# Optimization experiments

Hardware: AMD Instinct MI355X
Metric: run time of the kernel (lower is better)

Reference implementation:

```python
import jax, jax.numpy as jnp
import numpy as np
from jax import lax

B, L, ENC_IN, MARK = 8, 512, 7, 4
D_MODEL, EXPAND, D_STATE, D_CONV = 512, 2, 16, 4
D_INNER = D_MODEL * EXPAND
DT_RANK = int(np.ceil(D_MODEL / 16))  # 32
PRED_LEN, C_OUT = 96, 7


def _positional_embedding(seq_len, d_model):
    pos = jnp.arange(seq_len, dtype=jnp.float32)[:, None]
    div = jnp.exp(jnp.arange(0, d_model, 2, dtype=jnp.float32) * (-np.log(10000.0) / d_model))
    pe = jnp.zeros((seq_len, d_model), dtype=jnp.float32)
    pe = pe.at[:, 0::2].set(jnp.sin(pos * div))
    pe = pe.at[:, 1::2].set(jnp.cos(pos * div))
    return pe  # [L, d_model]


def setup_inputs() -> dict:
    key = jax.random.key(0)
    ks = jax.random.split(key, 20)
    s = 0.02
    inp = {
        "x_enc": jax.random.normal(ks[0], (B, L, ENC_IN), jnp.float32),
        "x_mark_enc": jax.random.normal(ks[1], (B, L, MARK), jnp.float32),
        "x_dec": jax.random.normal(ks[2], (B, 144, ENC_IN), jnp.float32),
        "x_mark_dec": jax.random.normal(ks[3], (B, 144, MARK), jnp.float32),
        # DataEmbedding params
        "token_conv_w": jax.random.normal(ks[4], (D_MODEL, ENC_IN, 3), jnp.float32) * s,
        "temporal_w": jax.random.normal(ks[5], (D_MODEL, MARK), jnp.float32) * s,
        # Mamba params
        "in_proj_w": jax.random.normal(ks[6], (2 * D_INNER, D_MODEL), jnp.float32) * s,
        "conv1d_w": jax.random.normal(ks[7], (D_INNER, 1, D_CONV), jnp.float32) * s,
        "conv1d_b": jnp.zeros((D_INNER,), jnp.float32),
        "x_proj_w": jax.random.normal(ks[8], (DT_RANK + 2 * D_STATE, D_INNER), jnp.float32) * s,
        "dt_proj_w": jax.random.normal(ks[9], (D_INNER, DT_RANK), jnp.float32) * s,
        "dt_proj_b": jax.random.normal(ks[10], (D_INNER,), jnp.float32) * s,
        "A_log": jnp.log(jnp.broadcast_to(jnp.arange(1, D_STATE + 1, dtype=jnp.float32), (D_INNER, D_STATE))),
        "D_param": jnp.ones((D_INNER,), jnp.float32),
        "out_proj_w": jax.random.normal(ks[11], (D_MODEL, D_INNER), jnp.float32) * s,
        # prediction head
        "head_w": jax.random.normal(ks[12], (PRED_LEN * C_OUT, D_MODEL), jnp.float32) * s,
        "head_b": jnp.zeros((PRED_LEN * C_OUT,), jnp.float32),
    }
    return inp


def reference(x_enc, x_mark_enc, x_dec, x_mark_dec, token_conv_w, temporal_w,
              in_proj_w, conv1d_w, conv1d_b, x_proj_w, dt_proj_w, dt_proj_b,
              A_log, D_param, out_proj_w, head_w, head_b):
    # --- instance normalization (mean/std detached as in torch) ---
    mean_enc = lax.stop_gradient(jnp.mean(x_enc, axis=1, keepdims=True))       # [B,1,C]
    xc = x_enc - mean_enc
    std_enc = lax.stop_gradient(jnp.sqrt(jnp.var(xc, axis=1, keepdims=True) + 1e-5))
    xn = xc / std_enc                                                          # [B,L,C]

    # --- DataEmbedding: circular conv token emb + timeF linear + sinusoidal PE ---
    xp = jnp.pad(xn, ((0, 0), (1, 1), (0, 0)), mode="wrap")                    # circular pad on L
    val = lax.conv_general_dilated(xp.transpose(0, 2, 1), token_conv_w, (1,), "VALID")  # [B,D,L]
    val = val.transpose(0, 2, 1)                                               # [B,L,D]
    temp = x_mark_enc @ temporal_w.T                                           # [B,L,D]
    x = val + temp + _positional_embedding(L, D_MODEL)[None]                   # [B,L,D]

    # --- Mamba block ---
    xz = x @ in_proj_w.T                                                       # [B,L,2*Di]
    x_part, z = jnp.split(xz, 2, axis=-1)
    # causal depthwise conv over time
    xt = jnp.pad(x_part.transpose(0, 2, 1), ((0, 0), (0, 0), (D_CONV - 1, 0)))
    xconv = lax.conv_general_dilated(xt, conv1d_w, (1,), "VALID",
                                     feature_group_count=D_INNER) + conv1d_b[None, :, None]
    u = jax.nn.silu(xconv.transpose(0, 2, 1))                                  # [B,L,Di]

    dbl = u @ x_proj_w.T                                                       # [B,L,dt_rank+2n]
    dt_low = dbl[..., :DT_RANK]
    Bm = dbl[..., DT_RANK:DT_RANK + D_STATE]                                   # [B,L,n]
    Cm = dbl[..., DT_RANK + D_STATE:]                                          # [B,L,n]
    dt = jax.nn.softplus(dt_low @ dt_proj_w.T + dt_proj_b)                     # [B,L,Di]

    A = -jnp.exp(A_log)                                                        # [Di,n]
    deltaA = jnp.exp(dt[..., None] * A)                                        # [B,L,Di,n]
    deltaBu = dt[..., None] * Bm[:, :, None, :] * u[..., None]                 # [B,L,Di,n]

    def step(h, inputs):
        dA_t, dBu_t, c_t = inputs                                              # [B,Di,n],[B,Di,n],[B,n]
        h = dA_t * h + dBu_t
        y_t = jnp.einsum("bdn,bn->bd", h, c_t)
        return h, y_t

    h0 = jnp.zeros((B, D_INNER, D_STATE), dtype=x.dtype)
    _, ys = lax.scan(step, h0, (deltaA.transpose(1, 0, 2, 3),
                                deltaBu.transpose(1, 0, 2, 3),
                                Cm.transpose(1, 0, 2)))
    y = ys.transpose(1, 0, 2) + u * D_param                                    # [B,L,Di]
    y = y * jax.nn.silu(z)
    x_out = y @ out_proj_w.T                                                   # [B,L,D]

    # --- prediction head on last hidden state ---
    last = x_out[:, -1, :]                                                     # [B,D]
    pred = (last @ head_w.T + head_b).reshape(-1, PRED_LEN, C_OUT)
    return pred * std_enc + mean_enc
```

## Files before the change

### kernel.cpp

```cpp
#include <hip/hip_runtime.h>
#include <hip/hip_bf16.h>
#include <math.h>

#define BB 8
#define LL 512
#define CIN 7
#define MARKN 4
#define DM 512
#define DI 1024
#define DSN 16
#define NOUTC 672
#define NTC 8

typedef unsigned short ushortT;
typedef __attribute__((ext_vector_type(8))) short short8v;
typedef __attribute__((ext_vector_type(4))) float f32x4;

__device__ __forceinline__ float bf2f(ushortT u){ return __uint_as_float(((unsigned)u)<<16); }
__device__ __forceinline__ ushortT f2bf(float f){ __hip_bfloat16 h = __float2bfloat16(f); return *(ushortT*)&h; }

__global__ __launch_bounds__(256) void k_prep(const float* __restrict__ w_in,
    const float* __restrict__ xpw, const float* __restrict__ xe,
    ushortT* __restrict__ wbf, ushortT* __restrict__ xpwbf,
    float* __restrict__ mean, float* __restrict__ stdv, float* __restrict__ xn){
  int blk = blockIdx.x, tid = threadIdx.x;
  if(blk < 1024){
    int i = (blk*256 + tid)*4;
    float4 v = *(const float4*)(w_in + i);
    ushort4 pk; pk.x=f2bf(v.x); pk.y=f2bf(v.y); pk.z=f2bf(v.z); pk.w=f2bf(v.w);
    *(ushort4*)(wbf + i) = pk;
  } else if(blk < 1088){
    int i = ((blk-1024)*256 + tid)*4;
    float4 v = *(const float4*)(xpw + i);
    ushort4 pk; pk.x=f2bf(v.x); pk.y=f2bf(v.y); pk.z=f2bf(v.z); pk.w=f2bf(v.w);
    *(ushort4*)(xpwbf + i) = pk;
  } else if(tid < 64){
    int bc = blk - 1088;
    int b = bc / CIN, c = bc % CIN;
    int t = tid;
    const float* base = xe + (b*LL)*CIN + c;
    float v[8]; float s = 0.f;
    #pragma unroll
    for(int i=0;i<8;i++){ v[i] = base[(t + i*64)*CIN]; s += v[i]; }
    #pragma unroll
    for(int o=32;o>=1;o>>=1) s += __shfl_down(s, o);
    float m = __shfl(s, 0) * (1.0f/LL);
    float vs = 0.f;
    #pragma unroll
    for(int i=0;i<8;i++){ float dv = v[i]-m; vs += dv*dv; }
    #pragma unroll
    for(int o=32;o>=1;o>>=1) vs += __shfl_down(vs, o);
    float var = __shfl(vs, 0) * (1.0f/LL);
    float sd = sqrtf(var + 1e-5f);
    float inv = 1.0f / sd;
    if(t == 0){ mean[bc] = m; stdv[bc] = sd; }
    float* xnb = xn + (b*LL)*CIN + c;
    #pragma unroll
    for(int i=0;i<8;i++) xnb[(t + i*64)*CIN] = (v[i]-m)*inv;
  }
}

__global__ __launch_bounds__(512) void k_embed(const float* __restrict__ xn,
    const float* __restrict__ xmark, const float* __restrict__ tw,
    const float* __restrict__ tpw, __hip_bfloat16* __restrict__ xo){
  __shared__ float sw[DM*21];
  __shared__ float sxr[10][CIN];
  __shared__ float smr[8][MARKN];
  int blk = blockIdx.x;
  int b = blk >> 6;
  int l0 = (blk & 63) << 3;
  int tid = threadIdx.x;
  for(int i=tid; i<DM*21; i+=512) sw[i] = tw[i];
  if(tid < 70){
    int r = tid / CIN, c = tid % CIN;
    int ls = (l0 - 1 + r + LL) % LL;
    sxr[r][c] = xn[(b*LL + ls)*CIN + c];
  } else if(tid >= 128 && tid < 160){
    int i2 = tid - 128; int r = i2 >> 2, m = i2 & 3;
    smr[r][m] = xmark[(b*LL + l0 + r)*MARKN + m];
  }
  __syncthreads();
  int d = tid;
  float wv[21];
  #pragma unroll
  for(int i=0;i<21;i++) wv[i] = sw[d*21 + i];
  float tv[4];
  #pragma unroll
  for(int m=0;m<4;m++) tv[m] = tpw[d*MARKN + m];
  float divv = expf((float)(2*(d>>1)) * (-0.0179889460390159843f));
  bool isodd = (d & 1) != 0;
  #pragma unroll
  for(int ll=0; ll<8; ll++){
    float acc = 0.f;
    #pragma unroll
    for(int c=0;c<CIN;c++){
      #pragma unroll
      for(int k=0;k<3;k++) acc += sxr[ll+k][c] * wv[c*3+k];
    }
    #pragma unroll
    for(int m=0;m<4;m++) acc += smr[ll][m] * tv[m];
    float ang = (float)(l0+ll) * divv;
    acc += isodd ? cosf(ang) : sinf(ang);
    xo[(size_t)(b*LL + l0 + ll)*DM + d] = __float2bfloat16(acc);
  }
}

__global__ __launch_bounds__(256) void k_inproj_mfma(const ushortT* __restrict__ A,
    const ushortT* __restrict__ Bw, ushortT* __restrict__ C){
  __shared__ ushortT Asl[2][128*64];
  __shared__ ushortT Bsl[2][128*64];
  int tid = threadIdx.x;
  int w = tid >> 6, l = tid & 63;
  int m0 = blockIdx.y * 128, n0 = blockIdx.x * 128;
  int wr = w >> 1, wc = w & 1;
  f32x4 acc[4][4] = {};
  int srow = l >> 3;
  int scolswz = ((l & 7) * 16) ^ (srow << 4);

#define IP_STAGE(bufi, kt) do{ \
    _Pragma("unroll") \
    for(int i=0;i<4;i++){ \
      int r0 = w*32 + i*8; \
      int r = r0 + srow; \
      const ushortT* gA = A + (size_t)(m0 + r)*512 + (kt)*64 + (scolswz>>1); \
      const ushortT* gB = Bw + (size_t)(n0 + r)*512 + (kt)*64 + (scolswz>>1); \
      __builtin_amdgcn_global_load_lds( \
        (const __attribute__((address_space(1))) unsigned int*)(const void*)gA, \
        (__attribute__((address_space(3))) unsigned int*)(void*)(Asl[bufi] + r0*64), 16, 0, 0); \
      __builtin_amdgcn_global_load_lds( \
        (const __attribute__((address_space(1))) unsigned int*)(const void*)gB, \
        (__attribute__((address_space(3))) unsigned int*)(void*)(Bsl[bufi] + r0*64), 16, 0, 0); \
    } }while(0)

  IP_STAGE(0, 0);
  __syncthreads();
  int cur = 0;
  for(int kt = 0; kt < 8; ++kt){
    if(kt < 7) IP_STAGE(cur^1, kt+1);
    #pragma unroll
    for(int kk=0;kk<2;kk++){
      short8v af[4], bfr[4];
      int cb = kk*64 + (l>>4)*16;
      #pragma unroll
      for(int mf=0;mf<4;mf++){
        int ar = wr*64 + mf*16 + (l&15);
        af[mf] = *(const short8v*)(Asl[cur] + ar*64 + ((cb ^ ((ar&7)<<4))>>1));
      }
      #pragma unroll
      for(int nf=0;nf<4;nf++){
        int br = wc*64 + nf*16 + (l&15);
        bfr[nf] = *(const short8v*)(Bsl[cur] + br*64 + ((cb ^ ((br&7)<<4))>>1));
      }
      #pragma unroll
      for(int mf=0;mf<4;mf++)
        #pragma unroll
        for(int nf=0;nf<4;nf++)
          acc[mf][nf] = __builtin_amdgcn_mfma_f32_16x16x32_bf16(af[mf], bfr[nf], acc[mf][nf], 0, 0, 0);
    }
    __syncthreads();
    cur ^= 1;
  }
#undef IP_STAGE
  #pragma unroll
  for(int mf=0;mf<4;mf++){
    int rbase = m0 + wr*64 + mf*16 + (l>>4)*4;
    #pragma unroll
    for(int nf=0;nf<4;nf++){
      int col = n0 + wc*64 + nf*16 + (l&15);
      #pragma unroll
      for(int r=0;r<4;r++)
        C[(size_t)(rbase+r)*1024 + col] = f2bf(acc[mf][nf][r]);
    }
  }
}

__global__ __launch_bounds__(1024) void k_dwconv(const ushortT* __restrict__ xpbf,
    const float* __restrict__ cw, const float* __restrict__ cb,
    ushortT* __restrict__ ubf){
  int blk = blockIdx.x;
  int b = blk >> 5, l0 = (blk & 31) * 16;
  int d = threadIdx.x;
  const float4 w4 = *(const float4*)(cw + d*4);
  float bias = cb[d];
  const ushortT* base = xpbf + (size_t)(b*LL + l0)*1024 + d;
  float x0=0.f, x1=0.f, x2=0.f;
  if(l0 > 0){
    x0 = bf2f(base[-3*1024]); x1 = bf2f(base[-2*1024]); x2 = bf2f(base[-1*1024]);
  }
  #pragma unroll
  for(int ll=0; ll<16; ++ll){
    float x3 = bf2f(base[(size_t)ll*1024]);
    float acc = bias + x0*w4.x + x1*w4.y + x2*w4.z + x3*w4.w;
    float s = acc / (1.f + __expf(-acc));
    ubf[(size_t)(b*LL + l0 + ll)*1024 + d] = f2bf(s);
    x0 = x1; x1 = x2; x2 = x3;
  }
}

__global__ __launch_bounds__(256) void k_xproj_mfma(const ushortT* __restrict__ A,
    const ushortT* __restrict__ Bw, float* __restrict__ C){
  __shared__ ushortT Asl[2][64*64];
  __shared__ ushortT Bsl[2][64*64];
  int tid = threadIdx.x;
  int w = tid >> 6, l = tid & 63;
  int m0 = blockIdx.x * 64;
  f32x4 acc[4] = {};
  int srow = l >> 3;
  int scol = ((l & 7) * 16) ^ (srow << 4);

#define XP_STAGE(bufi, kt) do{ \
    _Pragma("unroll") \
    for(int i=0;i<2;i++){ \
      int r0 = w*16 + i*8; \
      int r = r0 + srow; \
      const ushortT* gA = A + (size_t)(m0 + r)*1024 + (kt)*64 + (scol>>1); \
      const ushortT* gB = Bw + (size_t)r*1024 + (kt)*64 + (scol>>1); \
      __builtin_amdgcn_global_load_lds( \
        (const __attribute__((address_space(1))) unsigned int*)(const void*)gA, \
        (__attribute__((address_space(3))) unsigned int*)(void*)(Asl[bufi] + r0*64), 16, 0, 0); \
      __builtin_amdgcn_global_load_lds( \
        (const __attribute__((address_space(1))) unsigned int*)(const void*)gB, \
        (__attribute__((address_space(3))) unsigned int*)(void*)(Bsl[bufi] + r0*64), 16, 0, 0); \
    } }while(0)

  XP_STAGE(0, 0);
  __syncthreads();
  int cur = 0;
  for(int kt = 0; kt < 16; ++kt){
    if(kt < 15) XP_STAGE(cur^1, kt+1);
    #pragma unroll
    for(int kk=0;kk<2;kk++){
      int cb = kk*64 + (l>>4)*16;
      int ar = w*16 + (l&15);
      short8v af = *(const short8v*)(Asl[cur] + ar*64 + ((cb ^ ((ar&7)<<4))>>1));
      #pragma unroll
      for(int nf=0;nf<4;nf++){
        int br = nf*16 + (l&15);
        short8v bfv = *(const short8v*)(Bsl[cur] + br*64 + ((cb ^ ((br&7)<<4))>>1));
        acc[nf] = __builtin_amdgcn_mfma_f32_16x16x32_bf16(af, bfv, acc[nf], 0, 0, 0);
      }
    }
    __syncthreads();
    cur ^= 1;
  }
#undef XP_STAGE
  int rbase = m0 + w*16 + (l>>4)*4;
  #pragma unroll
  for(int nf=0;nf<4;nf++){
    int col = nf*16 + (l&15);
    #pragma unroll
    for(int r=0;r<4;r++)
      C[(size_t)(rbase+r)*64 + col] = acc[nf][r];
  }
}

__global__ __launch_bounds__(256) void k_scan_chunk(const float* __restrict__ dbl,
    const ushortT* __restrict__ ubf, const float* __restrict__ dtw,
    const float* __restrict__ dtb, const float* __restrict__ alog,
    float4* __restrict__ P4, float4* __restrict__ Q4){
  int tc = blockIdx.x;
  int dgrp = blockIdx.y;
  int b = blockIdx.z;
  int tid = threadIdx.x;
  int d = dgrp*256 + tid;
  __shared__ float sD[64][68];
  #pragma unroll
  for(int j=0;j<4;j++){
    int idx = j*256 + tid;
    int row = idx >> 4, q = idx & 15;
    float4 v = *(const float4*)(dbl + (size_t)(b*LL + tc*64 + row)*64 + q*4);
    *(float4*)(&sD[row][q*4]) = v;
  }
  float wdt[32];
  #pragma unroll
  for(int r4=0;r4<8;r4++){
    float4 v = *(const float4*)(dtw + (size_t)d*32 + r4*4);
    wdt[r4*4]=v.x; wdt[r4*4+1]=v.y; wdt[r4*4+2]=v.z; wdt[r4*4+3]=v.w;
  }
  float bias = dtb[d];
  float Ad[16];
  {
    float4 a0 = *(const float4*)(alog + d*16);
    float4 a1 = *(const float4*)(alog + d*16 + 4);
    float4 a2 = *(const float4*)(alog + d*16 + 8);
    float4 a3 = *(const float4*)(alog + d*16 + 12);
    Ad[0]=-__expf(a0.x); Ad[1]=-__expf(a0.y); Ad[2]=-__expf(a0.z); Ad[3]=-__expf(a0.w);
    Ad[4]=-__expf(a1.x); Ad[5]=-__expf(a1.y); Ad[6]=-__expf(a1.z); Ad[7]=-__expf(a1.w);
    Ad[8]=-__expf(a2.x); Ad[9]=-__expf(a2.y); Ad[10]=-__expf(a2.z); Ad[11]=-__expf(a2.w);
    Ad[12]=-__expf(a3.x); Ad[13]=-__expf(a3.y); Ad[14]=-__expf(a3.z); Ad[15]=-__expf(a3.w);
  }
  __syncthreads();
  float h[16];
  #pragma unroll
  for(int n=0;n<16;n++) h[n] = 0.f;
  float Ss = 0.f;
  const ushortT* up = ubf + (size_t)(b*LL + tc*64)*1024 + d;
  #pragma unroll 2
  for(int t=0;t<64;t++){
    float acc = bias;
    #pragma unroll
    for(int r=0;r<32;r++) acc += sD[t][r]*wdt[r];
    float dtv = (acc > 20.f) ? acc : __logf(1.f + __expf(acc));
    float uv = bf2f(up[(size_t)t*1024]);
    float wt = dtv * uv;
    Ss += dtv;
    #pragma unroll
    for(int n=0;n<16;n++){
      float e = __expf(dtv * Ad[n]);
      h[n] = h[n]*e + wt*sD[t][32+n];
    }
  }
  size_t base4 = (size_t)(tc*8 + b)*4*1024 + d;
  #pragma unroll
  for(int n4=0;n4<4;n4++){
    Q4[base4 + n4*1024] = make_float4(h[n4*4], h[n4*4+1], h[n4*4+2], h[n4*4+3]);
    P4[base4 + n4*1024] = make_float4(__expf(Ss*Ad[n4*4]), __expf(Ss*Ad[n4*4+1]),
                                      __expf(Ss*Ad[n4*4+2]), __expf(Ss*Ad[n4*4+3]));
  }
}

__global__ __launch_bounds__(64) void k_scan_combine(const float4* __restrict__ P4,
    const float4* __restrict__ Q4, const float* __restrict__ dbl,
    const ushortT* __restrict__ ubf, const ushortT* __restrict__ xbf,
    const ushortT* __restrict__ wbf, const float* __restrict__ Dp,
    float* __restrict__ yv){
  int gid = blockIdx.x*64 + threadIdx.x;
  int b = gid >> 10, d = gid & 1023;
  const ushortT* xr = xbf + (size_t)(b*LL + LL-1)*512;
  const ushortT* wr = wbf + (size_t)(1024 + d)*512;
  float zl = 0.f;
  for(int k=0;k<512;k+=8){
    short8v xv = *(const short8v*)(xr + k);
    short8v wv = *(const short8v*)(wr + k);
    #pragma unroll
    for(int j=0;j<8;j++) zl += bf2f((ushortT)xv[j])*bf2f((ushortT)wv[j]);
  }
  float h[16];
  #pragma unroll
  for(int n=0;n<16;n++) h[n] = 0.f;
  #pragma unroll
  for(int c=0;c<NTC;c++){
    size_t base4 = (size_t)(c*8 + b)*4*1024 + d;
    #pragma unroll
    for(int n4=0;n4<4;n4++){
      float4 pv = P4[base4 + n4*1024];
      float4 qv = Q4[base4 + n4*1024];
      h[n4*4+0] = pv.x*h[n4*4+0] + qv.x;
      h[n4*4+1] = pv.y*h[n4*4+1] + qv.y;
      h[n4*4+2] = pv.z*h[n4*4+2] + qv.z;
      h[n4*4+3] = pv.w*h[n4*4+3] + qv.w;
    }
  }
  const float* Crow = dbl + (size_t)(b*LL + LL-1)*64 + 48;
  float y = 0.f;
  #pragma unroll
  for(int n=0;n<16;n++) y += Crow[n]*h[n];
  float ul = bf2f(ubf[(size_t)(b*LL + LL-1)*1024 + d]);
  float sz = zl / (1.f + __expf(-zl));
  yv[b*1024 + d] = (y + ul*Dp[d]) * sz;
}

__global__ __launch_bounds__(256) void k_outproj(const float* __restrict__ yv,
    const float* __restrict__ W, float* __restrict__ xout){
  int tid = threadIdx.x;
  int j = blockIdx.x*8 + (tid>>5);
  int ks = tid & 31;
  float a[8] = {};
  #pragma unroll
  for(int t=0;t<8;t++){
    int k = ks*4 + t*128;
    float4 wv = *(const float4*)(W + (size_t)j*1024 + k);
    #pragma unroll
    for(int b=0;b<8;b++){
      float4 xv = *(const float4*)(yv + b*1024 + k);
      a[b] += xv.x*wv.x + xv.y*wv.y + xv.z*wv.z + xv.w*wv.w;
    }
  }
  #pragma unroll
  for(int b=0;b<8;b++){
    #pragma unroll
    for(int o=16;o>=1;o>>=1) a[b] += __shfl_xor(a[b], o);
  }
  if(ks==0){
    #pragma unroll
    for(int b=0;b<8;b++) xout[b*512 + j] = a[b];
  }
}

__global__ __launch_bounds__(256) void k_head(const float* __restrict__ xout,
    const float* __restrict__ W, const float* __restrict__ hb,
    const float* __restrict__ mean, const float* __restrict__ stdv,
    float* __restrict__ out){
  int tid = threadIdx.x;
  int o = blockIdx.x*8 + (tid>>5);
  int ks = tid & 31;
  float a[8] = {};
  #pragma unroll
  for(int t=0;t<4;t++){
    int k = ks*4 + t*128;
    float4 wv = *(const float4*)(W + (size_t)o*512 + k);
    #pragma unroll
    for(int b=0;b<8;b++){
      float4 xv = *(const float4*)(xout + b*512 + k);
      a[b] += xv.x*wv.x + xv.y*wv.y + xv.z*wv.z + xv.w*wv.w;
    }
  }
  #pragma unroll
  for(int b=0;b<8;b++){
    #pragma unroll
    for(int oo=16;oo>=1;oo>>=1) a[b] += __shfl_xor(a[b], oo);
  }
  if(ks==0){
    int c = o % 7;
    #pragma unroll
    for(int b=0;b<8;b++){
      float v = a[b] + hb[o];
      out[b*NOUTC + o] = v * stdv[b*CIN + c] + mean[b*CIN + c];
    }
  }
}

extern "C" void kernel_launch(void* const* d_in, const int* in_sizes, int n_in,
                              void* d_out, int out_size, void* d_ws, size_t ws_size,
                              hipStream_t stream) {
  const float* x_enc   = (const float*)d_in[0];
  const float* x_mark  = (const float*)d_in[1];
  const float* tconvw  = (const float*)d_in[4];
  const float* tempw   = (const float*)d_in[5];
  const float* inprojw = (const float*)d_in[6];
  const float* convw   = (const float*)d_in[7];
  const float* convb   = (const float*)d_in[8];
  const float* xprojw  = (const float*)d_in[9];
  const float* dtw     = (const float*)d_in[10];
  const float* dtb     = (const float*)d_in[11];
  const float* alog    = (const float*)d_in[12];
  const float* dpar    = (const float*)d_in[13];
  const float* outw    = (const float*)d_in[14];
  const float* headw   = (const float*)d_in[15];
  const float* headb   = (const float*)d_in[16];

  float* ws    = (float*)d_ws;
  float* mean  = ws;
  float* stdv  = ws + 64;
  float* xn    = ws + 128;
  ushortT* xbf = (ushortT*)(ws + 28800);
  ushortT* wbf = (ushortT*)(ws + 1077376);
  ushortT* xpwbf=(ushortT*)(ws + 1601664);
  ushortT* xpbf= (ushortT*)(ws + 1634432);
  ushortT* ubf = (ushortT*)(ws + 3731584);
  float* dbl   = ws + 5828736;
  float4* P4   = (float4*)(ws + 6090880);
  float4* Q4   = (float4*)(ws + 7139456);
  float* yv    = ws + 8188032;
  float* xout  = ws + 8196224;
  float* out   = (float*)d_out;

  k_prep  <<<1144, 256, 0, stream>>>(inprojw, xprojw, x_enc, wbf, xpwbf, mean, stdv, xn);
  k_embed <<<512, 512, 0, stream>>>(xn, x_mark, tconvw, tempw, (__hip_bfloat16*)xbf);
  k_inproj_mfma<<<dim3(8, 32), 256, 0, stream>>>(xbf, wbf, xpbf);
  k_dwconv<<<256, 1024, 0, stream>>>(xpbf, convw, convb, ubf);
  k_xproj_mfma<<<64, 256, 0, stream>>>(ubf, xpwbf, dbl);
  k_scan_chunk<<<dim3(NTC, 4, 8), 256, 0, stream>>>(dbl, ubf, dtw, dtb, alog, P4, Q4);
  k_scan_combine<<<128, 64, 0, stream>>>(P4, Q4, dbl, ubf, xbf, wbf, dpar, yv);
  k_outproj<<<64, 256, 0, stream>>>(yv, outw, xout);
  k_head  <<<84, 256, 0, stream>>>(xout, headw, headb, mean, stdv, out);
}
```

Before: 102.5 us.

## Fuse normalization into embedding kernel and split scan-combine across four lanes

Merges the prep and embed kernels into one launch. Each embed block recomputes the per-channel mean and std for its batch instead of writing a normalized intermediate buffer, which removes one launch and one global round trip. Weight conversion to bf16 now runs in the same grid. Separately, scan-combine gives each (b,d) unit four threads that each handle a quarter of the z dot product and the state dimension, then reduce with shuffles. This raises parallelism in a small latency-bound kernel, at the cost of redundant statistics computation in every embed block.

```diff
diff --git a/kernel.cpp b/kernel.cpp
--- a/kernel.cpp
+++ b/kernel.cpp
@@ -8,7 +8,6 @@
 #define MARKN 4
 #define DM 512
 #define DI 1024
-#define DSN 16
 #define NOUTC 672
 #define NTC 8
 
@@ -19,89 +18,86 @@
 __device__ __forceinline__ float bf2f(ushortT u){ return __uint_as_float(((unsigned)u)<<16); }
 __device__ __forceinline__ ushortT f2bf(float f){ __hip_bfloat16 h = __float2bfloat16(f); return *(ushortT*)&h; }
 
-__global__ __launch_bounds__(256) void k_prep(const float* __restrict__ w_in,
-    const float* __restrict__ xpw, const float* __restrict__ xe,
-    ushortT* __restrict__ wbf, ushortT* __restrict__ xpwbf,
-    float* __restrict__ mean, float* __restrict__ stdv, float* __restrict__ xn){
+__global__ __launch_bounds__(512) void k_prep_embed(const float* __restrict__ xe,
+    const float* __restrict__ xmark, const float* __restrict__ tw,
+    const float* __restrict__ tpw, const float* __restrict__ inprojw,
+    const float* __restrict__ xpw,
+    __hip_bfloat16* __restrict__ xo, ushortT* __restrict__ wbf,
+    ushortT* __restrict__ xpwbf, float* __restrict__ mean, float* __restrict__ stdv){
+  __shared__ float sw[DM*21];
+  __shared__ float sxr[10][CIN];
+  __shared__ float smr[8][MARKN];
+  __shared__ float sMean[8], sInv[8];
   int blk = blockIdx.x, tid = threadIdx.x;
-  if(blk < 1024){
-    int i = (blk*256 + tid)*4;
-    float4 v = *(const float4*)(w_in + i);
+  if(blk < 512){
+    int b = blk >> 6;
+    int l0 = (blk & 63) << 3;
+    int wv = tid >> 6, t2 = tid & 63;
+    if(wv < 7){
+      int c = wv;
+      const float* base = xe + (b*LL)*CIN + c;
+      float v[8]; float s = 0.f;
+      #pragma unroll
+      for(int i=0;i<8;i++){ v[i] = base[(t2 + i*64)*CIN]; s += v[i]; }
+      #pragma unroll
+      for(int o=32;o>=1;o>>=1) s += __shfl_down(s, o);
+      float m = __shfl(s, 0) * (1.0f/LL);
+      float vs = 0.f;
+      #pragma unroll
+      for(int i=0;i<8;i++){ float dv = v[i]-m; vs += dv*dv; }
+      #pragma unroll
+      for(int o=32;o>=1;o>>=1) vs += __shfl_down(vs, o);
+      float var = __shfl(vs, 0) * (1.0f/LL);
+      float sd = sqrtf(var + 1e-5f);
+      if(t2 == 0){
+        sMean[c] = m; sInv[c] = 1.0f/sd;
+        if(l0 == 0){ mean[b*CIN+c] = m; stdv[b*CIN+c] = sd; }
+      }
+    }
+    __syncthreads();
+    for(int i=tid; i<DM*21; i+=512) sw[i] = tw[i];
+    if(tid < 70){
+      int r = tid / CIN, c = tid % CIN;
+      int ls = (l0 - 1 + r + LL) % LL;
+      sxr[r][c] = (xe[(b*LL + ls)*CIN + c] - sMean[c]) * sInv[c];
+    } else if(tid >= 128 && tid < 160){
+      int i2 = tid - 128; int r = i2 >> 2, m = i2 & 3;
+      smr[r][m] = xmark[(b*LL + l0 + r)*MARKN + m];
+    }
+    __syncthreads();
+    int d = tid;
+    float wv2[21];
+    #pragma unroll
+    for(int i=0;i<21;i++) wv2[i] = sw[d*21 + i];
+    float tv[4];
+    #pragma unroll
+    for(int m=0;m<4;m++) tv[m] = tpw[d*MARKN + m];
+    float divv = expf((float)(2*(d>>1)) * (-0.0179889460390159843f));
+    bool isodd = (d & 1) != 0;
+    #pragma unroll
+    for(int ll=0; ll<8; ll++){
+      float acc = 0.f;
+      #pragma unroll
+      for(int c=0;c<CIN;c++){
+        #pragma unroll
+        for(int k=0;k<3;k++) acc += sxr[ll+k][c] * wv2[c*3+k];
+      }
+      #pragma unroll
+      for(int m=0;m<4;m++) acc += smr[ll][m] * tv[m];
+      float ang = (float)(l0+ll) * divv;
+      acc += isodd ? cosf(ang) : sinf(ang);
+      xo[(size_t)(b*LL + l0 + ll)*DM + d] = __float2bfloat16(acc);
+    }
+  } else if(blk < 1024){
+    int i = ((blk-512)*512 + tid)*4;
+    float4 v = *(const float4*)(inprojw + i);
     ushort4 pk; pk.x=f2bf(v.x); pk.y=f2bf(v.y); pk.z=f2bf(v.z); pk.w=f2bf(v.w);
     *(ushort4*)(wbf + i) = pk;
-  } else if(blk < 1088){
-    int i = ((blk-1024)*256 + tid)*4;
+  } else {
+    int i = ((blk-1024)*512 + tid)*4;
     float4 v = *(const float4*)(xpw + i);
     ushort4 pk; pk.x=f2bf(v.x); pk.y=f2bf(v.y); pk.z=f2bf(v.z); pk.w=f2bf(v.w);
     *(ushort4*)(xpwbf + i) = pk;
-  } else if(tid < 64){
-    int bc = blk - 1088;
-    int b = bc / CIN, c = bc % CIN;
-    int t = tid;
-    const float* base = xe + (b*LL)*CIN + c;
-    float v[8]; float s = 0.f;
-    #pragma unroll
-    for(int i=0;i<8;i++){ v[i] = base[(t + i*64)*CIN]; s += v[i]; }
-    #pragma unroll
-    for(int o=32;o>=1;o>>=1) s += __shfl_down(s, o);
-    float m = __shfl(s, 0) * (1.0f/LL);
-    float vs = 0.f;
-    #pragma unroll
-    for(int i=0;i<8;i++){ float dv = v[i]-m; vs += dv*dv; }
-    #pragma unroll
-    for(int o=32;o>=1;o>>=1) vs += __shfl_down(vs, o);
-    float var = __shfl(vs, 0) * (1.0f/LL);
-    float sd = sqrtf(var + 1e-5f);
-    float inv = 1.0f / sd;
-    if(t == 0){ mean[bc] = m; stdv[bc] = sd; }
-    float* xnb = xn + (b*LL)*CIN + c;
-    #pragma unroll
-    for(int i=0;i<8;i++) xnb[(t + i*64)*CIN] = (v[i]-m)*inv;
-  }
-}
-
-__global__ __launch_bounds__(512) void k_embed(const float* __restrict__ xn,
-    const float* __restrict__ xmark, const float* __restrict__ tw,
-    const float* __restrict__ tpw, __hip_bfloat16* __restrict__ xo){
-  __shared__ float sw[DM*21];
-  __shared__ float sxr[10][CIN];
-  __shared__ float smr[8][MARKN];
-  int blk = blockIdx.x;
-  int b = blk >> 6;
-  int l0 = (blk & 63) << 3;
-  int tid = threadIdx.x;
-  for(int i=tid; i<DM*21; i+=512) sw[i] = tw[i];
-  if(tid < 70){
-    int r = tid / CIN, c = tid % CIN;
-    int ls = (l0 - 1 + r + LL) % LL;
-    sxr[r][c] = xn[(b*LL + ls)*CIN + c];
-  } else if(tid >= 128 && tid < 160){
-    int i2 = tid - 128; int r = i2 >> 2, m = i2 & 3;
-    smr[r][m] = xmark[(b*LL + l0 + r)*MARKN + m];
-  }
-  __syncthreads();
-  int d = tid;
-  float wv[21];
-  #pragma unroll
-  for(int i=0;i<21;i++) wv[i] = sw[d*21 + i];
-  float tv[4];
-  #pragma unroll
-  for(int m=0;m<4;m++) tv[m] = tpw[d*MARKN + m];
-  float divv = expf((float)(2*(d>>1)) * (-0.0179889460390159843f));
-  bool isodd = (d & 1) != 0;
-  #pragma unroll
-  for(int ll=0; ll<8; ll++){
-    float acc = 0.f;
-    #pragma unroll
-    for(int c=0;c<CIN;c++){
-      #pragma unroll
-      for(int k=0;k<3;k++) acc += sxr[ll+k][c] * wv[c*3+k];
-    }
-    #pragma unroll
-    for(int m=0;m<4;m++) acc += smr[ll][m] * tv[m];
-    float ang = (float)(l0+ll) * divv;
-    acc += isodd ? cosf(ang) : sinf(ang);
-    xo[(size_t)(b*LL + l0 + ll)*DM + d] = __float2bfloat16(acc);
   }
 }
 
@@ -297,10 +293,10 @@
   const ushortT* up = ubf + (size_t)(b*LL + tc*64)*1024 + d;
   #pragma unroll 2
   for(int t=0;t<64;t++){
-    float acc = bias;
-    #pragma unroll
-    for(int r=0;r<32;r++) acc += sD[t][r]*wdt[r];
-    float dtv = (acc > 20.f) ? acc : __logf(1.f + __expf(acc));
+    float a2 = bias;
+    #pragma unroll
+    for(int r=0;r<32;r++) a2 += sD[t][r]*wdt[r];
+    float dtv = (a2 > 20.f) ? a2 : __logf(1.f + __expf(a2));
     float uv = bf2f(up[(size_t)t*1024]);
     float wt = dtv * uv;
     Ss += dtv;
@@ -319,45 +315,47 @@
   }
 }
 
-__global__ __launch_bounds__(64) void k_scan_combine(const float4* __restrict__ P4,
+__global__ __launch_bounds__(256) void k_scan_combine(const float4* __restrict__ P4,
     const float4* __restrict__ Q4, const float* __restrict__ dbl,
     const ushortT* __restrict__ ubf, const ushortT* __restrict__ xbf,
     const ushortT* __restrict__ wbf, const float* __restrict__ Dp,
     float* __restrict__ yv){
-  int gid = blockIdx.x*64 + threadIdx.x;
-  int b = gid >> 10, d = gid & 1023;
-  const ushortT* xr = xbf + (size_t)(b*LL + LL-1)*512;
-  const ushortT* wr = wbf + (size_t)(1024 + d)*512;
+  int tid = threadIdx.x;
+  int unit = blockIdx.x*64 + (tid>>2);
+  int sub = tid & 3;
+  int b = unit >> 10, d = unit & 1023;
+  const ushortT* xr = xbf + (size_t)(b*LL + LL-1)*512 + sub*128;
+  const ushortT* wr = wbf + (size_t)(1024 + d)*512 + sub*128;
   float zl = 0.f;
-  for(int k=0;k<512;k+=8){
+  #pragma unroll
+  for(int k=0;k<128;k+=8){
     short8v xv = *(const short8v*)(xr + k);
     short8v wv = *(const short8v*)(wr + k);
     #pragma unroll
     for(int j=0;j<8;j++) zl += bf2f((ushortT)xv[j])*bf2f((ushortT)wv[j]);
   }
-  float h[16];
-  #pragma unroll
-  for(int n=0;n<16;n++) h[n] = 0.f;
+  zl += __shfl_xor(zl, 1);
+  zl += __shfl_xor(zl, 2);
+  float h0=0.f, h1=0.f, h2=0.f, h3=0.f;
   #pragma unroll
   for(int c=0;c<NTC;c++){
-    size_t base4 = (size_t)(c*8 + b)*4*1024 + d;
-    #pragma unroll
-    for(int n4=0;n4<4;n4++){
-      float4 pv = P4[base4 + n4*1024];
-      float4 qv = Q4[base4 + n4*1024];
-      h[n4*4+0] = pv.x*h[n4*4+0] + qv.x;
-      h[n4*4+1] = pv.y*h[n4*4+1] + qv.y;
-      h[n4*4+2] = pv.z*h[n4*4+2] + qv.z;
-      h[n4*4+3] = pv.w*h[n4*4+3] + qv.w;
-    }
-  }
-  const float* Crow = dbl + (size_t)(b*LL + LL-1)*64 + 48;
-  float y = 0.f;
-  #pragma unroll
-  for(int n=0;n<16;n++) y += Crow[n]*h[n];
-  float ul = bf2f(ubf[(size_t)(b*LL + LL-1)*1024 + d]);
-  float sz = zl / (1.f + __expf(-zl));
-  yv[b*1024 + d] = (y + ul*Dp[d]) * sz;
+    size_t idx = (size_t)(c*8 + b)*4*1024 + sub*1024 + d;
+    float4 pv = P4[idx];
+    float4 qv = Q4[idx];
+    h0 = pv.x*h0 + qv.x;
+    h1 = pv.y*h1 + qv.y;
+    h2 = pv.z*h2 + qv.z;
+    h3 = pv.w*h3 + qv.w;
+  }
+  const float* Crow = dbl + (size_t)(b*LL + LL-1)*64 + 48 + sub*4;
+  float y = Crow[0]*h0 + Crow[1]*h1 + Crow[2]*h2 + Crow[3]*h3;
+  y += __shfl_xor(y, 1);
+  y += __shfl_xor(y, 2);
+  if(sub == 0){
+    float ul = bf2f(ubf[(size_t)(b*LL + LL-1)*1024 + d]);
+    float sz = zl / (1.f + __expf(-zl));
+    yv[b*1024 + d] = (y + ul*Dp[d]) * sz;
+  }
 }
 
 __global__ __launch_bounds__(256) void k_outproj(const float* __restrict__ yv,
@@ -442,26 +440,25 @@
   float* ws    = (float*)d_ws;
   float* mean  = ws;
   float* stdv  = ws + 64;
-  float* xn    = ws + 128;
-  ushortT* xbf = (ushortT*)(ws + 28800);
-  ushortT* wbf = (ushortT*)(ws + 1077376);
-  ushortT* xpwbf=(ushortT*)(ws + 1601664);
-  ushortT* xpbf= (ushortT*)(ws + 1634432);
-  ushortT* ubf = (ushortT*)(ws + 3731584);
-  float* dbl   = ws + 5828736;
-  float4* P4   = (float4*)(ws + 6090880);
-  float4* Q4   = (float4*)(ws + 7139456);
-  float* yv    = ws + 8188032;
-  float* xout  = ws + 8196224;
+  ushortT* xbf = (ushortT*)(ws + 128);
+  ushortT* wbf = (ushortT*)(ws + 1048704);
+  ushortT* xpwbf=(ushortT*)(ws + 1572992);
+  ushortT* xpbf= (ushortT*)(ws + 1605760);
+  ushortT* ubf = (ushortT*)(ws + 3702912);
+  float* dbl   = ws + 5800064;
+  float4* P4   = (float4*)(ws + 6062208);
+  float4* Q4   = (float4*)(ws + 7110784);
+  float* yv    = ws + 8159360;
+  float* xout  = ws + 8167552;
   float* out   = (float*)d_out;
 
-  k_prep  <<<1144, 256, 0, stream>>>(inprojw, xprojw, x_enc, wbf, xpwbf, mean, stdv, xn);
-  k_embed <<<512, 512, 0, stream>>>(xn, x_mark, tconvw, tempw, (__hip_bfloat16*)xbf);
+  k_prep_embed<<<1056, 512, 0, stream>>>(x_enc, x_mark, tconvw, tempw, inprojw, xprojw,
+                                         (__hip_bfloat16*)xbf, wbf, xpwbf, mean, stdv);
   k_inproj_mfma<<<dim3(8, 32), 256, 0, stream>>>(xbf, wbf, xpbf);
   k_dwconv<<<256, 1024, 0, stream>>>(xpbf, convw, convb, ubf);
   k_xproj_mfma<<<64, 256, 0, stream>>>(ubf, xpwbf, dbl);
   k_scan_chunk<<<dim3(NTC, 4, 8), 256, 0, stream>>>(dbl, ubf, dtw, dtb, alog, P4, Q4);
-  k_scan_combine<<<128, 64, 0, stream>>>(P4, Q4, dbl, ubf, xbf, wbf, dpar, yv);
+  k_scan_combine<<<128, 256, 0, stream>>>(P4, Q4, dbl, ubf, xbf, wbf, dpar, yv);
   k_outproj<<<64, 256, 0, stream>>>(yv, outw, xout);
   k_head  <<<84, 256, 0, stream>>>(xout, headw, headb, mean, stdv, out);
 }
```

Measured after the change: 94.21 us. -8.1%, faster.
